# Kernel optimization log

Measured on AMD Instinct MI355X. Metric: run time of the kernel, lower is better.

Reference implementation:

```python
import jax, jax.numpy as jnp
import numpy as np

# ---- static config (mirrors TALoss(num_classes=80, reg_max=16, strides=[8,16,32])) ----
B, M, NC, REG_MAX = 32, 20, 80, 16
STRIDES = (8, 16, 32)
HW = ((80, 80), (40, 40), (20, 20))          # feature map sizes for 640x640 input
NO = REG_MAX * 4 + NC                         # 144 channels per head
A = sum(h * w for h, w in HW)                 # 8400 anchors
TOPK, ALPHA, BETA = 10, 0.5, 6.0
BOX_G, CLS_G, DFL_G = 7.5, 0.5, 1.5
EPS = 1e-9


def setup_inputs() -> dict:
    key = jax.random.key(0)
    ks = jax.random.split(key, 6)
    feats = {f"feat{i}": jax.random.normal(ks[i], (B, NO, h, w), jnp.float32)
             for i, (h, w) in enumerate(HW)}
    # targets: (N,6) rows of (img_idx, class, cx, cy, w, h), normalized, 20 boxes/image, sorted by image
    img_idx = jnp.repeat(jnp.arange(B, dtype=jnp.float32), M)
    cls = jax.random.randint(ks[3], (B * M,), 0, NC).astype(jnp.float32)
    cxy = jax.random.uniform(ks[4], (B * M, 2), minval=0.2, maxval=0.8)
    wh = jax.random.uniform(ks[5], (B * M, 2), minval=0.05, maxval=0.3)
    targets = jnp.concatenate([img_idx[:, None], cls[:, None], cxy, wh], axis=1)
    return {**feats, "targets": targets}


def _make_anchors():
    pts, strs = [], []
    for (h, w), s in zip(HW, STRIDES):
        sx = jnp.arange(w, dtype=jnp.float32) + 0.5
        sy = jnp.arange(h, dtype=jnp.float32) + 0.5
        gy, gx = jnp.meshgrid(sy, sx, indexing="ij")
        pts.append(jnp.stack([gx, gy], -1).reshape(-1, 2))
        strs.append(jnp.full((h * w, 1), float(s), jnp.float32))
    return jnp.concatenate(pts), jnp.concatenate(strs)   # (A,2), (A,1)


def _ciou(b1, b2, eps=1e-7):
    # b1, b2: broadcastable xyxy boxes (..., 4) -> CIoU (...,)
    b1x1, b1y1, b1x2, b1y2 = b1[..., 0], b1[..., 1], b1[..., 2], b1[..., 3]
    b2x1, b2y1, b2x2, b2y2 = b2[..., 0], b2[..., 1], b2[..., 2], b2[..., 3]
    w1, h1 = b1x2 - b1x1, b1y2 - b1y1 + eps
    w2, h2 = b2x2 - b2x1, b2y2 - b2y1 + eps
    inter = (jnp.clip(jnp.minimum(b1x2, b2x2) - jnp.maximum(b1x1, b2x1), 0)
             * jnp.clip(jnp.minimum(b1y2, b2y2) - jnp.maximum(b1y1, b2y1), 0))
    union = w1 * h1 + w2 * h2 - inter + eps
    iou = inter / union
    cw = jnp.maximum(b1x2, b2x2) - jnp.minimum(b1x1, b2x1)
    ch = jnp.maximum(b1y2, b2y2) - jnp.minimum(b1y1, b2y1)
    c2 = cw ** 2 + ch ** 2 + eps
    rho2 = ((b2x1 + b2x2 - b1x1 - b1x2) ** 2 + (b2y1 + b2y2 - b1y1 - b1y2) ** 2) / 4.0
    v = (4.0 / np.pi ** 2) * (jnp.arctan(w2 / h2) - jnp.arctan(w1 / h1)) ** 2
    a = jax.lax.stop_gradient(v / (v - iou + (1.0 + eps)))   # torch: computed under no_grad
    return iou - (rho2 / c2 + v * a)


def _assign(pd_scores, pd_bboxes, anc, gt_labels, gt_bboxes, mask_gt):
    """TaskAlignedAssigner. pd_scores (B,A,NC) sigmoid-ed, pd_bboxes (B,A,4) image units,
    anc (A,2) image units, gt_labels (B,M), gt_bboxes (B,M,4), mask_gt (B,M) float."""
    # anchors inside each gt box -> (B,M,A)
    lt = anc[None, None, :, :] - gt_bboxes[:, :, None, :2]
    rb = gt_bboxes[:, :, None, 2:] - anc[None, None, :, :]
    mask_in = (jnp.concatenate([lt, rb], -1).min(-1) > EPS).astype(jnp.float32)
    mask = mask_in * mask_gt[..., None]                      # (B,M,A) candidate mask
    overlaps = jnp.clip(_ciou(gt_bboxes[:, :, None, :], pd_bboxes[:, None, :, :]), 0) * mask
    labels = gt_labels.astype(jnp.int32)                     # (B,M)
    # scores of each gt's class at every anchor: (B,M,A)
    bbox_scores = jnp.take_along_axis(pd_scores.transpose(0, 2, 1),
                                      jnp.broadcast_to(labels[:, :, None], (B, M, A)), axis=1) * mask
    align = (bbox_scores ** ALPHA) * (overlaps ** BETA)      # (B,M,A), already zero off-mask
    # top-k anchors per gt
    _, idxs = jax.lax.top_k(align, TOPK)                     # (B,M,K)
    idxs = jnp.where(mask_gt[..., None] > 0, idxs, 0)
    cnt = jax.nn.one_hot(idxs, A, dtype=jnp.float32).sum(-2)  # (B,M,A)
    mask_topk = jnp.where(cnt > 1, 0.0, cnt)
    mask_pos = mask_topk * mask
    # resolve anchors matched to multiple gts: keep the max-overlap gt
    fg = mask_pos.sum(1)                                     # (B,A)
    is_max = jnp.moveaxis(jax.nn.one_hot(overlaps.argmax(1), M, dtype=jnp.float32), -1, 1)  # (B,M,A)
    mask_pos = jnp.where(fg[:, None, :] > 1, is_max, mask_pos)
    fg = mask_pos.sum(1)
    tgt_idx = mask_pos.argmax(1)                             # (B,A)
    t_labels = jnp.take_along_axis(labels, tgt_idx, 1)       # (B,A)
    t_bboxes = jnp.take_along_axis(gt_bboxes, tgt_idx[..., None], 1)  # (B,A,4)
    fg_b = (fg > 0).astype(jnp.float32)
    t_scores = jax.nn.one_hot(t_labels, NC, dtype=jnp.float32) * fg_b[..., None]
    # normalize scores: align * (max overlap per gt) / (max align per gt)
    align_pos = align * mask_pos
    pos_align = align_pos.max(-1, keepdims=True)             # (B,M,1)
    pos_over = (overlaps * mask_pos).max(-1, keepdims=True)
    norm = (align_pos * pos_over / (pos_align + EPS)).max(1)  # (B,A)
    return t_bboxes, t_scores * norm[..., None], fg_b


def _forward(feat0, feat1, feat2, targets):
    feats = [feat0, feat1, feat2]
    pred = jnp.concatenate([f.reshape(B, NO, -1) for f in feats], axis=2)
    pred_distri = pred[:, :REG_MAX * 4].transpose(0, 2, 1)   # (B,A,64)
    pred_scores = pred[:, REG_MAX * 4:].transpose(0, 2, 1)   # (B,A,NC)
    anc, stride_t = _make_anchors()
    img_h, img_w = HW[0][0] * STRIDES[0], HW[0][1] * STRIDES[0]
    scale = jnp.array([img_w, img_h, img_w, img_h], jnp.float32)
    # ---- preprocess targets (N,6) -> padded (B,M,5), xywh*scale -> xyxy ----
    idx = targets[:, 0].astype(jnp.int32)
    pos = jnp.arange(targets.shape[0]) - jnp.searchsorted(idx, idx, side="left")
    out = jnp.zeros((B, M, 5), jnp.float32).at[idx, pos].set(targets[:, 1:])
    gt_labels = out[..., 0]
    xywh = out[..., 1:5] * scale
    gt_bboxes = jnp.concatenate([xywh[..., :2] - xywh[..., 2:] / 2,
                                 xywh[..., :2] + xywh[..., 2:] / 2], -1)
    mask_gt = (gt_bboxes.sum(-1) > 0).astype(jnp.float32)    # (B,M)
    # ---- DFL bbox decode (feature-map units) ----
    proj = jnp.arange(REG_MAX, dtype=jnp.float32)
    dist = jax.nn.softmax(pred_distri.reshape(B, A, 4, REG_MAX), -1) @ proj  # (B,A,4) ltrb
    pred_bboxes = jnp.concatenate([anc - dist[..., :2], anc + dist[..., 2:]], -1)
    # ---- task-aligned assignment (on detached preds, image units) ----
    pd_scores = jax.lax.stop_gradient(jax.nn.sigmoid(pred_scores))
    pd_bboxes = jax.lax.stop_gradient(pred_bboxes) * stride_t
    target_bboxes, target_scores, fg_mask = _assign(pd_scores, pd_bboxes, anc * stride_t,
                                                    gt_labels, gt_bboxes, mask_gt)
    target_bboxes = target_bboxes / stride_t
    tss = jnp.maximum(target_scores.sum(), 1.0)
    # ---- BCE-with-logits classification loss (pos_weight=1) ----
    x, t = pred_scores, target_scores
    bce = jnp.maximum(x, 0) - x * t + jnp.log1p(jnp.exp(-jnp.abs(x)))
    loss_cls = bce.sum() / tss
    # ---- CIoU box loss + DFL, weighted by per-anchor target score sum on fg ----
    weight = target_scores.sum(-1) * fg_mask                 # (B,A)
    iou = _ciou(pred_bboxes, target_bboxes)
    loss_box = ((1.0 - iou) * weight).sum() / tss
    tltrb = jnp.clip(jnp.concatenate([anc - target_bboxes[..., :2],
                                      target_bboxes[..., 2:] - anc], -1),
                     0, REG_MAX - 1 - 0.01)                  # (B,A,4)
    logp = jax.nn.log_softmax(pred_distri.reshape(B, A, 4, REG_MAX), -1)
    tl = tltrb.astype(jnp.int32)
    wl = (tl + 1).astype(jnp.float32) - tltrb
    nll_l = -jnp.take_along_axis(logp, tl[..., None], -1)[..., 0]
    nll_r = -jnp.take_along_axis(logp, (tl + 1)[..., None], -1)[..., 0]
    dfl = (nll_l * wl + nll_r * (1.0 - wl)).mean(-1)         # (B,A)
    loss_dfl = (dfl * weight).sum() / tss
    losses = jnp.stack([loss_box * BOX_G, loss_cls * CLS_G, loss_dfl * DFL_G])
    return losses.sum() * B, jax.lax.stop_gradient(losses)


def reference(feat0, feat1, feat2, targets):
    return _forward(feat0, feat1, feat2, targets)
```

## Files before the change

kernel.cpp:

```cpp
#include <hip/hip_runtime.h>
#include <math.h>

constexpr int BB  = 32;
constexpr int MM  = 20;
constexpr int NCC = 80;
constexpr int RM  = 16;
constexpr int NOC = 144;
constexpr int AT  = 8400;
constexpr int TK  = 10;
constexpr int BA  = BB * AT;
constexpr int BM  = BB * MM;
constexpr int MAXPOS = BM * TK;
constexpr int NSLOT = 1024;
constexpr float EPS_A = 1e-9f;
constexpr float VCOEF = 0.40528473456935108577551785283891f;

constexpr int NBOX0 = BB * 6400 / 256;
constexpr int NBOX1 = BB * 1600 / 256;
constexpr int NBOX2 = BB * 400 / 256;
constexpr int NBOX  = NBOX0 + NBOX1 + NBOX2;
constexpr int NBCE  = 2048;
constexpr unsigned C0F4 = 80 * 6400 / 4;
constexpr unsigned C1F4 = 80 * 1600 / 4;
constexpr unsigned C2F4 = 80 * 400 / 4;
constexpr unsigned CBF4 = C0F4 + C1F4 + C2F4;
constexpr unsigned NF4  = (unsigned)BB * CBF4;

struct Lvl { const float* f; int o, w, hw; float s; };

__device__ inline Lvl level_of(int a, const float* f0, const float* f1, const float* f2){
  Lvl L;
  if (a < 6400)      { L.f = f0; L.o = a;        L.w = 80; L.hw = 6400; L.s = 8.f;  }
  else if (a < 8000) { L.f = f1; L.o = a - 6400; L.w = 40; L.hw = 1600; L.s = 16.f; }
  else               { L.f = f2; L.o = a - 8000; L.w = 20; L.hw = 400;  L.s = 32.f; }
  return L;
}

__device__ inline float frcp(float x){ return __builtin_amdgcn_rcpf(x); }

__device__ inline float fast_atan(float x){
  float ax = fabsf(x);
  bool big = ax > 1.f;
  float z = big ? frcp(ax) : ax;
  float z2 = z * z;
  float p = fmaf(z2, -0.0117212f, 0.0526533f);
  p = fmaf(z2, p, -0.1164329f);
  p = fmaf(z2, p, 0.1935435f);
  p = fmaf(z2, p, -0.3326235f);
  p = fmaf(z2, p, 0.9999773f);
  float r = z * p;
  r = big ? 1.57079632679f - r : r;
  return copysignf(r, x);
}

__device__ inline float ciou_f(float b1x1,float b1y1,float b1x2,float b1y2,
                               float b2x1,float b2y1,float b2x2,float b2y2){
  const float eps = 1e-7f;
  float w1 = b1x2 - b1x1, h1 = b1y2 - b1y1 + eps;
  float w2 = b2x2 - b2x1, h2 = b2y2 - b2y1 + eps;
  float iw = fmaxf(fminf(b1x2, b2x2) - fmaxf(b1x1, b2x1), 0.f);
  float ih = fmaxf(fminf(b1y2, b2y2) - fmaxf(b1y1, b2y1), 0.f);
  float inter = iw * ih;
  float uni = w1 * h1 + w2 * h2 - inter + eps;
  float iou = inter * frcp(uni);
  float cw = fmaxf(b1x2, b2x2) - fminf(b1x1, b2x1);
  float ch = fmaxf(b1y2, b2y2) - fminf(b1y1, b2y1);
  float c2 = cw * cw + ch * ch + eps;
  float dx = b2x1 + b2x2 - b1x1 - b1x2;
  float dy = b2y1 + b2y2 - b1y1 - b1y2;
  float rho2 = (dx * dx + dy * dy) * 0.25f;
  float r1 = w1 * frcp(h1), r2 = w2 * frcp(h2);
  float dat = fast_atan((r2 - r1) * frcp(fmaf(r1, r2, 1.f)));
  float v = VCOEF * dat * dat;
  float alpha = v * frcp(v - iou + (1.0f + eps));
  return iou - (rho2 * frcp(c2) + v * alpha);
}

__device__ inline unsigned long long shfl_xor_u64(unsigned long long v, int mask){
  int lo = __shfl_xor((int)(unsigned)(v & 0xFFFFFFFFull), mask);
  int hi = __shfl_xor((int)(unsigned)(v >> 32), mask);
  return ((unsigned long long)(unsigned)hi << 32) | (unsigned)lo;
}

__device__ inline float softplus4(float4 v){
  float s = fmaxf(v.x, 0.f) + __logf(1.f + __expf(-fabsf(v.x)));
  s += fmaxf(v.y, 0.f) + __logf(1.f + __expf(-fabsf(v.y)));
  s += fmaxf(v.z, 0.f) + __logf(1.f + __expf(-fabsf(v.z)));
  s += fmaxf(v.w, 0.f) + __logf(1.f + __expf(-fabsf(v.w)));
  return s;
}

template<int HW, int W, int AOFF>
__device__ inline void decode_anchor(const float* __restrict__ f, int u,
                                     float4* __restrict__ pbox,
                                     float4* __restrict__ lseg,
                                     unsigned* __restrict__ mpos){
  int b = u / HW, o = u - b * HW;
  const float* base = f + (size_t)b * NOC * HW + o;
  float d[4], ls[4];
#pragma unroll
  for (int side = 0; side < 4; side++){
    float x[16];
#pragma unroll
    for (int j = 0; j < 16; j++)
      x[j] = base[(size_t)((side * 16 + j) * HW)];
    float mx = x[0];
#pragma unroll
    for (int j = 1; j < 16; j++) mx = fmaxf(mx, x[j]);
    float sm = 0.f, dt = 0.f;
#pragma unroll
    for (int j = 0; j < 16; j++){
      float e = __expf(x[j] - mx);
      sm += e; dt = fmaf(e, (float)j, dt);
    }
    d[side]  = dt * frcp(sm);
    ls[side] = mx + __logf(sm);
  }
  int iy = o / W;
  float ax = (float)(o - iy * W) + 0.5f;
  float ay = (float)iy + 0.5f;
  int gi = b * AT + AOFF + o;
  pbox[gi] = make_float4(ax - d[0], ay - d[1], ax + d[2], ay + d[3]);
  lseg[gi] = make_float4(ls[0], ls[1], ls[2], ls[3]);
  mpos[gi] = 0u;
}

__global__ __launch_bounds__(256) void k_feat2(
    const float* __restrict__ f0, const float* __restrict__ f1,
    const float* __restrict__ f2, const float* __restrict__ tgt,
    float4* __restrict__ pbox, float4* __restrict__ lse,
    unsigned* __restrict__ mpos, double* __restrict__ bce_part,
    float* __restrict__ out5, float* __restrict__ gtbox,
    int* __restrict__ gtlab, float* __restrict__ gtmask,
    int* __restrict__ pa_i, int* __restrict__ po_i,
    int* __restrict__ topk_arr, double* __restrict__ acc){
  __shared__ float red[4];
  int blk = blockIdx.x;
  int tid = threadIdx.x;
  if (blk < NBOX){
    if (blk < NBOX0){
      decode_anchor<6400, 80, 0>(f0, blk * 256 + tid, pbox, lse, mpos);
    } else if (blk < NBOX0 + NBOX1){
      decode_anchor<1600, 40, 6400>(f1, (blk - NBOX0) * 256 + tid, pbox, lse, mpos);
    } else {
      decode_anchor<400, 20, 8000>(f2, (blk - NBOX0 - NBOX1) * 256 + tid, pbox, lse, mpos);
    }
  } else if (blk < NBOX + NBCE){
    int bi = blk - NBOX;
    float sp = 0.f;
    for (unsigned i = (unsigned)bi * 256u + (unsigned)tid; i < NF4;
         i += (unsigned)NBCE * 256u){
      unsigned b = i / CBF4;
      unsigned r = i - b * CBF4;
      const float4* p;
      if (r < C0F4)
        p = (const float4*)(f0) + (size_t)b * (NOC * 6400 / 4) + (64 * 6400 / 4) + r;
      else if (r < C0F4 + C1F4)
        p = (const float4*)(f1) + (size_t)b * (NOC * 1600 / 4) + (64 * 1600 / 4) + (r - C0F4);
      else
        p = (const float4*)(f2) + (size_t)b * (NOC * 400 / 4) + (64 * 400 / 4) + (r - C0F4 - C1F4);
      sp += softplus4(*p);
    }
    for (int off = 32; off; off >>= 1) sp += __shfl_down(sp, off);
    int wid = tid >> 6, lid = tid & 63;
    if (lid == 0) red[wid] = sp;
    __syncthreads();
    if (tid == 0) bce_part[bi] = (double)(red[0] + red[1] + red[2] + red[3]);
  } else {
    for (int i = tid; i < BM * 5; i += 256) out5[i] = 0.f;
    for (int i = tid; i < MAXPOS; i += 256) topk_arr[i] = -1;
    for (int i = tid; i < BM; i += 256){ pa_i[i] = 0; po_i[i] = 0; }
    if (tid < 8) acc[tid] = 0.0;
    __syncthreads();
    for (int t = tid; t < BM; t += 256){
      int img = (int)tgt[t * 6 + 0];
      int j = t;
      while (j > 0 && (int)tgt[(j - 1) * 6 + 0] == img) j--;
      int pos = t - j;
      if (img >= 0 && img < BB && pos < MM){
        for (int k = 0; k < 5; k++)
          out5[(img * MM + pos) * 5 + k] = tgt[t * 6 + 1 + k];
      }
    }
    __syncthreads();
    for (int t = tid; t < BM; t += 256){
      float lab = out5[t * 5 + 0];
      float cx = out5[t * 5 + 1] * 640.f;
      float cy = out5[t * 5 + 2] * 640.f;
      float w  = out5[t * 5 + 3] * 640.f;
      float h  = out5[t * 5 + 4] * 640.f;
      float x1 = cx - w * 0.5f, y1 = cy - h * 0.5f;
      float x2 = cx + w * 0.5f, y2 = cy + h * 0.5f;
      gtbox[t * 4 + 0] = x1; gtbox[t * 4 + 1] = y1;
      gtbox[t * 4 + 2] = x2; gtbox[t * 4 + 3] = y2;
      gtlab[t] = (int)lab;
      gtmask[t] = ((x1 + y1 + x2 + y2) > 0.f) ? 1.f : 0.f;
    }
  }
}

__global__ __launch_bounds__(256) void k_align(
    const float* __restrict__ f0, const float* __restrict__ f1,
    const float* __restrict__ f2, const float4* __restrict__ pbox,
    const float* __restrict__ gtbox, const int* __restrict__ gtlab,
    const float* __restrict__ gtmask,
    unsigned* __restrict__ mpos, int* __restrict__ topk_arr){
  int pair = blockIdx.x;
  int b = pair / MM, m = pair % MM;
  if (gtmask[pair] <= 0.f) return;
  int tid = threadIdx.x;
  float gx1 = gtbox[pair * 4 + 0], gy1 = gtbox[pair * 4 + 1];
  float gx2 = gtbox[pair * 4 + 2], gy2 = gtbox[pair * 4 + 3];
  int lab = gtlab[pair];
  __shared__ float s_val[NSLOT];
  __shared__ int   s_anc[NSLOT];
  __shared__ unsigned long long s_red[4];
  __shared__ int   s_win[TK];
  int base = 0;

#define PROC_LEVEL(FPTR, W, HW, AOFF, S)                                      \
  {                                                                           \
    const float s_ = (S); const float inv_ = 1.f / (S);                       \
    int x0 = max(0, (int)floorf(gx1 * inv_ - 0.5f));                          \
    int x1 = min((W) - 1, (int)ceilf(gx2 * inv_ - 0.5f));                     \
    int y0 = max(0, (int)floorf(gy1 * inv_ - 0.5f));                          \
    int y1 = min((W) - 1, (int)ceilf(gy2 * inv_ - 0.5f));                     \
    int nxx = x1 - x0 + 1, nyy = y1 - y0 + 1;                                 \
    if (nxx > 0 && nyy > 0){                                                  \
      int ntot = nxx * nyy;                                                   \
      unsigned magic = 0xFFFFFFFFu / (unsigned)nxx + 1u;                      \
      const float* clsrow = (FPTR) + (size_t)b * NOC * (HW)                   \
                            + (size_t)(4 * RM + lab) * (HW);                  \
      for (int t = tid; t < ntot; t += 256){                                  \
        int slot = base + t;                                                  \
        if (slot >= NSLOT) break;                                             \
        int iy = (int)(((unsigned long long)(unsigned)t * magic) >> 32);      \
        int ix = t - iy * nxx + x0;                                           \
        iy += y0;                                                             \
        float ax = ((float)ix + 0.5f) * s_;                                   \
        float ay = ((float)iy + 0.5f) * s_;                                   \
        float mn = fminf(fminf(ax - gx1, ay - gy1),                           \
                         fminf(gx2 - ax, gy2 - ay));                          \
        int o = iy * (W) + ix;                                                \
        int a = (AOFF) + o;                                                   \
        float aln = -1.f;                                                     \
        if (mn > EPS_A){                                                      \
          float4 pb = pbox[b * AT + a];                                       \
          float c = ciou_f(gx1, gy1, gx2, gy2,                                \
                           pb.x * s_, pb.y * s_, pb.z * s_, pb.w * s_);       \
          float ovl = fmaxf(c, 0.f);                                          \
          if (ovl > 0.f){                                                     \
            float xv = clsrow[o];                                             \
            float sc = frcp(1.f + __expf(-xv));                               \
            float o2 = ovl * ovl;                                             \
            aln = sqrtf(sc) * (o2 * o2 * o2);                                 \
          }                                                                   \
        }                                                                     \
        s_val[slot] = aln;                                                    \
        s_anc[slot] = a;                                                      \
      }                                                                       \
      base += ntot;                                                           \
    }                                                                         \
  }

  PROC_LEVEL(f0, 80, 6400, 0, 8.f)
  PROC_LEVEL(f1, 40, 1600, 6400, 16.f)
  PROC_LEVEL(f2, 20, 400, 8000, 32.f)
#undef PROC_LEVEL

  __syncthreads();
  int total = min(base, NSLOT);
  int wid = tid >> 6, lid = tid & 63;
  for (int r = 0; r < TK; r++){
    unsigned long long key = 0ULL;
    for (int i = tid; i < total; i += 256){
      float v = s_val[i];
      if (v > 0.f){
        unsigned long long k2 =
            ((unsigned long long)__float_as_uint(v) << 32) |
            (unsigned long long)(0xFFFFFFFFu - (unsigned)i);
        key = key > k2 ? key : k2;
      }
    }
    for (int xm = 1; xm < 64; xm <<= 1){
      unsigned long long o = shfl_xor_u64(key, xm);
      key = key > o ? key : o;
    }
    if (lid == 0) s_red[wid] = key;
    __syncthreads();
    if (tid == 0){
      unsigned long long k = s_red[0];
      k = k > s_red[1] ? k : s_red[1];
      k = k > s_red[2] ? k : s_red[2];
      k = k > s_red[3] ? k : s_red[3];
      if (k){
        int slot = (int)(0xFFFFFFFFu - (unsigned)(k & 0xFFFFFFFFull));
        s_win[r] = s_anc[slot];
        s_val[slot] = -1.f;
      } else s_win[r] = -1;
    }
    __syncthreads();
  }
  if (tid < TK){
    int a = s_win[tid];
    topk_arr[pair * TK + tid] = a;
    if (a >= 0) atomicOr(&mpos[(size_t)b * AT + a], 1u << m);
  }
}

__global__ __launch_bounds__(256) void k_resolve(
    const float* __restrict__ f0, const float* __restrict__ f1,
    const float* __restrict__ f2, const float4* __restrict__ pbox,
    const float* __restrict__ gtbox, const int* __restrict__ gtlab,
    const float* __restrict__ gtmask, const unsigned* __restrict__ mpos,
    const int* __restrict__ topk_arr,
    unsigned char* __restrict__ resm, float* __restrict__ resaln,
    int* __restrict__ pa_i, int* __restrict__ po_i){
  int i = blockIdx.x * 256 + threadIdx.x;
  int a = topk_arr[i];
  if (a < 0) return;
  int pair = i / TK;
  int b = pair / MM, m = pair % MM;
  unsigned bits = mpos[(size_t)b * AT + a];
  if (m != __ffs(bits) - 1) return;
  Lvl L = level_of(a, f0, f1, f2);
  float ax = ((float)(L.o % L.w) + 0.5f) * L.s;
  float ay = ((float)(L.o / L.w) + 0.5f) * L.s;
  float4 pb = pbox[b * AT + a];
  float px1 = pb.x * L.s, py1 = pb.y * L.s, px2 = pb.z * L.s, py2 = pb.w * L.s;
  int mr; float ovl;
  if (__popc(bits) > 1){
    float best = -1.f; int bm = 0;
    for (int mm = 0; mm < MM; mm++){
      float v = 0.f;
      if (gtmask[b * MM + mm] > 0.f){
        float x1 = gtbox[(b * MM + mm) * 4 + 0], y1 = gtbox[(b * MM + mm) * 4 + 1];
        float x2 = gtbox[(b * MM + mm) * 4 + 2], y2 = gtbox[(b * MM + mm) * 4 + 3];
        float mn = fminf(fminf(ax - x1, ay - y1), fminf(x2 - ax, y2 - ay));
        if (mn > EPS_A)
          v = fmaxf(ciou_f(x1, y1, x2, y2, px1, py1, px2, py2), 0.f);
      }
      if (v > best){ best = v; bm = mm; }
    }
    mr = bm; ovl = fmaxf(best, 0.f);
  } else {
    mr = m;
    float x1 = gtbox[(b * MM + mr) * 4 + 0], y1 = gtbox[(b * MM + mr) * 4 + 1];
    float x2 = gtbox[(b * MM + mr) * 4 + 2], y2 = gtbox[(b * MM + mr) * 4 + 3];
    ovl = fmaxf(ciou_f(x1, y1, x2, y2, px1, py1, px2, py2), 0.f);
  }
  int lab = gtlab[b * MM + mr];
  float xv = L.f[(size_t)b * NOC * L.hw + (size_t)(4 * RM + lab) * L.hw + L.o];
  float sc = frcp(1.f + __expf(-xv));
  float o2 = ovl * ovl;
  float aln = sqrtf(sc) * (o2 * o2 * o2);
  size_t gi = (size_t)b * AT + a;
  resm[gi] = (unsigned char)mr;
  resaln[gi] = aln;
  atomicMax(&pa_i[b * MM + mr], __float_as_int(aln));
  atomicMax(&po_i[b * MM + mr], __float_as_int(ovl));
}

__global__ __launch_bounds__(256) void k_final(
    const float* __restrict__ f0, const float* __restrict__ f1,
    const float* __restrict__ f2,
    const float4* __restrict__ pbox, const float4* __restrict__ lse,
    const float* __restrict__ gtbox, const int* __restrict__ gtlab,
    const int* __restrict__ pa_i, const int* __restrict__ po_i,
    const unsigned* __restrict__ mpos, const int* __restrict__ topk_arr,
    const unsigned char* __restrict__ resm, const float* __restrict__ resaln,
    double* __restrict__ acc){
  int i = blockIdx.x * 256 + threadIdx.x;
  float w_ = 0.f, clsp = 0.f, boxp = 0.f, dflp = 0.f;
  int a = topk_arr[i];
  if (a >= 0){
    int pair = i / TK;
    int b = pair / MM, m = pair % MM;
    unsigned bits = mpos[(size_t)b * AT + a];
    if (m == __ffs(bits) - 1){
      size_t gi = (size_t)b * AT + a;
      int mr = (int)resm[gi];
      float aln = resaln[gi];
      float pa = __int_as_float(pa_i[b * MM + mr]);
      float po = __int_as_float(po_i[b * MM + mr]);
      w_ = aln * po * frcp(pa + EPS_A);
      Lvl L = level_of(a, f0, f1, f2);
      const float* base = L.f + (size_t)b * NOC * L.hw + L.o;
      float ax = (float)(L.o % L.w) + 0.5f;
      float ay = (float)(L.o / L.w) + 0.5f;
      float inv_s = frcp(L.s);
      float tx1 = gtbox[(b * MM + mr) * 4 + 0] * inv_s, ty1 = gtbox[(b * MM + mr) * 4 + 1] * inv_s;
      float tx2 = gtbox[(b * MM + mr) * 4 + 2] * inv_s, ty2 = gtbox[(b * MM + mr) * 4 + 3] * inv_s;
      float4 pb = pbox[b * AT + a];
      float iou = ciou_f(pb.x, pb.y, pb.z, pb.w, tx1, ty1, tx2, ty2);
      boxp = (1.f - iou) * w_;
      float4 L4 = lse[b * AT + a];
      float lsv[4] = { L4.x, L4.y, L4.z, L4.w };
      float tv[4] = { ax - tx1, ay - ty1, tx2 - ax, ty2 - ay };
      float dfl = 0.f;
#pragma unroll
      for (int s4 = 0; s4 < 4; s4++){
        float t = fminf(fmaxf(tv[s4], 0.f), (float)(RM - 1) - 0.01f);
        int tl = (int)t;
        float wl = (float)(tl + 1) - t;
        float xl = base[(size_t)(s4 * RM + tl) * L.hw];
        float xr = base[(size_t)(s4 * RM + tl + 1) * L.hw];
        dfl += (lsv[s4] - xl) * wl + (lsv[s4] - xr) * (1.f - wl);
      }
      dflp = dfl * 0.25f * w_;
      int lab = gtlab[b * MM + mr];
      clsp = base[(size_t)(4 * RM + lab) * L.hw] * w_;
    }
  }
  __shared__ float red[4][4];
  float vals[4] = { w_, clsp, boxp, dflp };
  int wid = threadIdx.x >> 6, lid = threadIdx.x & 63;
#pragma unroll
  for (int j = 0; j < 4; j++){
    float v = vals[j];
    for (int off = 32; off; off >>= 1) v += __shfl_down(v, off);
    if (lid == 0) red[wid][j] = v;
  }
  __syncthreads();
  if (threadIdx.x == 0){
    float t0 = 0.f, t1 = 0.f, t2 = 0.f, t3 = 0.f;
    for (int w2 = 0; w2 < 4; w2++){
      t0 += red[w2][0]; t1 += red[w2][1]; t2 += red[w2][2]; t3 += red[w2][3];
    }
    atomicAdd(&acc[0], (double)t0);
    atomicAdd(&acc[1], (double)t1);
    atomicAdd(&acc[2], (double)t2);
    atomicAdd(&acc[3], (double)t3);
  }
}

__global__ void k_out(const double* __restrict__ acc,
                      const double* __restrict__ bce_part,
                      float* __restrict__ out){
  __shared__ double sd[256];
  double s = 0.0;
  for (int i = threadIdx.x; i < NBCE; i += 256) s += bce_part[i];
  sd[threadIdx.x] = s;
  __syncthreads();
  for (int off = 128; off; off >>= 1){
    if (threadIdx.x < off) sd[threadIdx.x] += sd[threadIdx.x + off];
    __syncthreads();
  }
  if (threadIdx.x == 0){
    double bce_sum = sd[0];
    double tss = acc[0] > 1.0 ? acc[0] : 1.0;
    double loss_box = acc[2] / tss;
    double loss_cls = (bce_sum - acc[1]) / tss;
    double loss_dfl = acc[3] / tss;
    float l0 = (float)(loss_box * 7.5);
    float l1 = (float)(loss_cls * 0.5);
    float l2 = (float)(loss_dfl * 1.5);
    out[0] = (l0 + l1 + l2) * 32.f;
    out[1] = l0;
    out[2] = l1;
    out[3] = l2;
  }
}

extern "C" void kernel_launch(void* const* d_in, const int* in_sizes, int n_in,
                              void* d_out, int out_size, void* d_ws, size_t ws_size,
                              hipStream_t stream) {
  const float* f0 = (const float*)d_in[0];
  const float* f1 = (const float*)d_in[1];
  const float* f2 = (const float*)d_in[2];
  const float* tg = (const float*)d_in[3];
  float* out = (float*)d_out;

  char* w = (char*)d_ws;
  size_t off = 0;
  auto alloc = [&](size_t bytes) -> void* {
    void* p = w + off;
    off += (bytes + 255) & ~(size_t)255;
    return p;
  };
  float4*        pbox    = (float4*)       alloc((size_t)BA * 16);
  float4*        lse     = (float4*)       alloc((size_t)BA * 16);
  float*         gtbox   = (float*)        alloc((size_t)BM * 16);
  int*           gtlab   = (int*)          alloc((size_t)BM * 4);
  float*         gtmask  = (float*)        alloc((size_t)BM * 4);
  float*         out5    = (float*)        alloc((size_t)BM * 20);
  unsigned*      mpos    = (unsigned*)     alloc((size_t)BA * 4);
  int*           topk_arr= (int*)          alloc((size_t)MAXPOS * 4);
  unsigned char* resm    = (unsigned char*)alloc((size_t)BA);
  float*         resaln  = (float*)        alloc((size_t)BA * 4);
  int*           pa      = (int*)          alloc((size_t)BM * 4);
  int*           po      = (int*)          alloc((size_t)BM * 4);
  double*        acc     = (double*)       alloc(8 * 8);
  double*        bcep    = (double*)       alloc((size_t)NBCE * 8);

  k_feat2<<<NBOX + NBCE + 1, 256, 0, stream>>>(f0, f1, f2, tg, pbox, lse, mpos, bcep,
                                               out5, gtbox, gtlab, gtmask, pa, po,
                                               topk_arr, acc);
  k_align<<<BM, 256, 0, stream>>>(f0, f1, f2, pbox, gtbox, gtlab, gtmask, mpos, topk_arr);
  k_resolve<<<MAXPOS / 256, 256, 0, stream>>>(f0, f1, f2, pbox, gtbox, gtlab, gtmask,
                                              mpos, topk_arr, resm, resaln, pa, po);
  k_final<<<MAXPOS / 256, 256, 0, stream>>>(f0, f1, f2, pbox, lse, gtbox, gtlab,
                                            pa, po, mpos, topk_arr, resm, resaln, acc);
  k_out<<<1, 256, 0, stream>>>(acc, bcep, out);
}
```

Baseline: 247.7 us.

## Fuse softplus BCE reduction into per-anchor decode blocks

The separate grid of BCE blocks that streamed the class channels with float4 loads is removed. Each decode thread now also reads its anchor's 80 class logits and accumulates softplus, writing one partial per decode block. This cuts launched blocks and the separate pass scheduling, but class loads become scalar strided loads per channel instead of float4, and per-thread work and register pressure rise. Launch bounds now request 4 blocks per SM.

After: 249.7 us. Within noise of the previous version (+0.8%).

```diff
diff --git a/kernel.cpp b/kernel.cpp
--- a/kernel.cpp
+++ b/kernel.cpp
@@ -19,12 +19,6 @@
 constexpr int NBOX1 = BB * 1600 / 256;
 constexpr int NBOX2 = BB * 400 / 256;
 constexpr int NBOX  = NBOX0 + NBOX1 + NBOX2;
-constexpr int NBCE  = 2048;
-constexpr unsigned C0F4 = 80 * 6400 / 4;
-constexpr unsigned C1F4 = 80 * 1600 / 4;
-constexpr unsigned C2F4 = 80 * 400 / 4;
-constexpr unsigned CBF4 = C0F4 + C1F4 + C2F4;
-constexpr unsigned NF4  = (unsigned)BB * CBF4;
 
 struct Lvl { const float* f; int o, w, hw; float s; };
 
@@ -82,21 +76,18 @@
   return ((unsigned long long)(unsigned)hi << 32) | (unsigned)lo;
 }
 
-__device__ inline float softplus4(float4 v){
-  float s = fmaxf(v.x, 0.f) + __logf(1.f + __expf(-fabsf(v.x)));
-  s += fmaxf(v.y, 0.f) + __logf(1.f + __expf(-fabsf(v.y)));
-  s += fmaxf(v.z, 0.f) + __logf(1.f + __expf(-fabsf(v.z)));
-  s += fmaxf(v.w, 0.f) + __logf(1.f + __expf(-fabsf(v.w)));
-  return s;
+__device__ inline float softplus1(float x){
+  return fmaxf(x, 0.f) + __logf(1.f + __expf(-fabsf(x)));
 }
 
 template<int HW, int W, int AOFF>
-__device__ inline void decode_anchor(const float* __restrict__ f, int u,
-                                     float4* __restrict__ pbox,
-                                     float4* __restrict__ lseg,
-                                     unsigned* __restrict__ mpos){
+__device__ inline float fused_tile(const float* __restrict__ f, int u,
+                                   float4* __restrict__ pbox,
+                                   float4* __restrict__ lseg,
+                                   unsigned* __restrict__ mpos){
   int b = u / HW, o = u - b * HW;
   const float* base = f + (size_t)b * NOC * HW + o;
+
   float d[4], ls[4];
 #pragma unroll
   for (int side = 0; side < 4; side++){
@@ -123,9 +114,23 @@
   pbox[gi] = make_float4(ax - d[0], ay - d[1], ax + d[2], ay + d[3]);
   lseg[gi] = make_float4(ls[0], ls[1], ls[2], ls[3]);
   mpos[gi] = 0u;
-}
-
-__global__ __launch_bounds__(256) void k_feat2(
+
+  const float* cbase = base + (size_t)(4 * RM) * HW;
+  float sp = 0.f;
+#pragma unroll
+  for (int jj = 0; jj < NCC; jj += 8){
+    float x[8];
+#pragma unroll
+    for (int j = 0; j < 8; j++)
+      x[j] = cbase[(size_t)((jj + j) * HW)];
+#pragma unroll
+    for (int j = 0; j < 8; j++)
+      sp += softplus1(x[j]);
+  }
+  return sp;
+}
+
+__global__ __launch_bounds__(256, 4) void k_feat3(
     const float* __restrict__ f0, const float* __restrict__ f1,
     const float* __restrict__ f2, const float* __restrict__ tgt,
     float4* __restrict__ pbox, float4* __restrict__ lse,
@@ -138,34 +143,19 @@
   int blk = blockIdx.x;
   int tid = threadIdx.x;
   if (blk < NBOX){
+    float sp;
     if (blk < NBOX0){
-      decode_anchor<6400, 80, 0>(f0, blk * 256 + tid, pbox, lse, mpos);
+      sp = fused_tile<6400, 80, 0>(f0, blk * 256 + tid, pbox, lse, mpos);
     } else if (blk < NBOX0 + NBOX1){
-      decode_anchor<1600, 40, 6400>(f1, (blk - NBOX0) * 256 + tid, pbox, lse, mpos);
+      sp = fused_tile<1600, 40, 6400>(f1, (blk - NBOX0) * 256 + tid, pbox, lse, mpos);
     } else {
-      decode_anchor<400, 20, 8000>(f2, (blk - NBOX0 - NBOX1) * 256 + tid, pbox, lse, mpos);
-    }
-  } else if (blk < NBOX + NBCE){
-    int bi = blk - NBOX;
-    float sp = 0.f;
-    for (unsigned i = (unsigned)bi * 256u + (unsigned)tid; i < NF4;
-         i += (unsigned)NBCE * 256u){
-      unsigned b = i / CBF4;
-      unsigned r = i - b * CBF4;
-      const float4* p;
-      if (r < C0F4)
-        p = (const float4*)(f0) + (size_t)b * (NOC * 6400 / 4) + (64 * 6400 / 4) + r;
-      else if (r < C0F4 + C1F4)
-        p = (const float4*)(f1) + (size_t)b * (NOC * 1600 / 4) + (64 * 1600 / 4) + (r - C0F4);
-      else
-        p = (const float4*)(f2) + (size_t)b * (NOC * 400 / 4) + (64 * 400 / 4) + (r - C0F4 - C1F4);
-      sp += softplus4(*p);
+      sp = fused_tile<400, 20, 8000>(f2, (blk - NBOX0 - NBOX1) * 256 + tid, pbox, lse, mpos);
     }
     for (int off = 32; off; off >>= 1) sp += __shfl_down(sp, off);
     int wid = tid >> 6, lid = tid & 63;
     if (lid == 0) red[wid] = sp;
     __syncthreads();
-    if (tid == 0) bce_part[bi] = (double)(red[0] + red[1] + red[2] + red[3]);
+    if (tid == 0) bce_part[blk] = (double)(red[0] + red[1] + red[2] + red[3]);
   } else {
     for (int i = tid; i < BM * 5; i += 256) out5[i] = 0.f;
     for (int i = tid; i < MAXPOS; i += 256) topk_arr[i] = -1;
@@ -439,7 +429,7 @@
                       float* __restrict__ out){
   __shared__ double sd[256];
   double s = 0.0;
-  for (int i = threadIdx.x; i < NBCE; i += 256) s += bce_part[i];
+  for (int i = threadIdx.x; i < NBOX; i += 256) s += bce_part[i];
   sd[threadIdx.x] = s;
   __syncthreads();
   for (int off = 128; off; off >>= 1){
@@ -491,11 +481,11 @@
   int*           pa      = (int*)          alloc((size_t)BM * 4);
   int*           po      = (int*)          alloc((size_t)BM * 4);
   double*        acc     = (double*)       alloc(8 * 8);
-  double*        bcep    = (double*)       alloc((size_t)NBCE * 8);
-
-  k_feat2<<<NBOX + NBCE + 1, 256, 0, stream>>>(f0, f1, f2, tg, pbox, lse, mpos, bcep,
-                                               out5, gtbox, gtlab, gtmask, pa, po,
-                                               topk_arr, acc);
+  double*        bcep    = (double*)       alloc((size_t)NBOX * 8);
+
+  k_feat3<<<NBOX + 1, 256, 0, stream>>>(f0, f1, f2, tg, pbox, lse, mpos, bcep,
+                                        out5, gtbox, gtlab, gtmask, pa, po,
+                                        topk_arr, acc);
   k_align<<<BM, 256, 0, stream>>>(f0, f1, f2, pbox, gtbox, gtlab, gtmask, mpos, topk_arr);
   k_resolve<<<MAXPOS / 256, 256, 0, stream>>>(f0, f1, f2, pbox, gtbox, gtlab, gtmask,
                                               mpos, topk_arr, resm, resaln, pa, po);
```
